# Kernel tuning notes

Measured on AMD Instinct MI355X. Metric: run time of the kernel, lower is better.

The kernel has to match this reference:

```python
import jax, jax.numpy as jnp
import numpy as np

S, B, R, H, TOP, CHL = 512, 32, 8, 128, 3, 19
I = CHL + 1  # GRU input size after null-channel concat


def setup_inputs() -> dict:
    key = jax.random.key(0)
    ks = jax.random.split(key, 12)
    f = lambda k, shp, sc=0.05: jax.random.normal(k, shp, dtype=jnp.float32) * sc
    return {
        "x": f(ks[0], (B, CHL, S), 1.0),
        "Wih": f(ks[1], (R, 3 * H, I)),      # per-rim GRU input weights (torch order r,z,n)
        "Whh": f(ks[2], (R, 3 * H, H)),      # per-rim GRU hidden weights
        "Qir_w": f(ks[3], (H, H)),
        "Qir_b": f(ks[4], (H,)),
        "Kir_w": f(ks[5], (H, S)),
        "Vir_w": f(ks[6], (H, S)),
        "Qrr_w": f(ks[7], (H, H)),
        "Krr_w": f(ks[8], (H, H)),
        "Vrr_w": f(ks[9], (H, H)),
    }


def reference(x, Wih, Whh, Qir_w, Qir_b, Kir_w, Vir_w, Qrr_w, Krr_w, Vrr_w):
    Bn = x.shape[0]
    # prepend null channel, reshape to (S, B, I)
    xc = jnp.concatenate([jnp.zeros((Bn, 1, x.shape[2]), x.dtype), x], axis=1)
    xs = jnp.transpose(xc, (2, 0, 1))  # (S, B, I)

    # ---- per-rim GRU (no bias), torch gate order (r, z, n) ----
    x_proj = jnp.einsum('sbi,rgi->srbg', xs, Wih)  # (S, R, B, 3H)

    def step(hprev, xp):
        hp = jnp.einsum('rbh,rgh->rbg', hprev, Whh)
        xr, xz, xn = jnp.split(xp, 3, axis=-1)
        hr, hz, hn = jnp.split(hp, 3, axis=-1)
        r = jax.nn.sigmoid(xr + hr)
        z = jax.nn.sigmoid(xz + hz)
        n = jnp.tanh(xn + r * hn)
        hnew = (1.0 - z) * n + z * hprev
        return hnew, hnew

    h0 = jnp.zeros((R, Bn, H), x.dtype)
    _, hs = jax.lax.scan(step, h0, x_proj)      # (S, R, B, H)
    h = jnp.transpose(hs, (1, 0, 2, 3))          # (R, S, B, H)

    # ---- stage one: input attention + rim competition ----
    x_bis = jnp.transpose(xs, (1, 2, 0))         # (B, I, S)
    q = jnp.einsum('rsbh,oh->rsbo', h, Qir_w) + Qir_b
    k = jnp.einsum('bis,os->bio', x_bis, Kir_w)
    v = jnp.einsum('bis,os->bio', x_bis, Vir_w)
    qk = jnp.einsum('rsbh,bih->sbri', q, k) / (H ** 0.5)
    soft = jax.nn.softmax(qk, axis=3)            # (S, B, R, I)
    idx = jax.lax.top_k(-soft[..., 0], TOP)[1]   # (S, B, TOP)
    mask = jnp.sum(jax.nn.one_hot(idx, R, dtype=jnp.float32), axis=-2)[..., None]  # (S,B,R,1)
    mask = jax.lax.stop_gradient(mask)
    qkv = jnp.einsum('sbri,bih->sbrh', soft, v)  # (S, B, R, H)

    # NoGrad: forward identity, backward grad*mask
    h1 = qkv * mask + jax.lax.stop_gradient(qkv * (1.0 - mask))

    # ---- stage two: rim-rim attention, masked ----
    q2 = jnp.einsum('sbrh,oh->sbro', h1, Qrr_w)
    k2 = jnp.einsum('sbrh,oh->sbro', h1, Krr_w)
    v2 = jnp.einsum('sbrh,oh->sbro', h1, Vrr_w)
    qk2 = jnp.einsum('sbrh,sbch->sbrc', q2, k2)  # (S, B, R, R), no scaling (as in source)
    soft2 = jax.nn.softmax(qk2, axis=3) * mask
    out = h1 + jnp.einsum('sbrc,sbch->sbrh', soft2, v2)
    return out * mask
```

## Files before the change

kernel.cpp:

```cpp
#include <hip/hip_runtime.h>
#include <math.h>


typedef float v2f __attribute__((ext_vector_type(2)));

#define PKF(acc, w, h) \
    asm("v_pk_fma_f32 %0, %1, %2, %0" : "+v"(acc) : "v"(w), "v"(h))

__global__ __launch_bounds__(256) void kPro1(const float* __restrict__ Kir,
        const float* __restrict__ Vir, const float* __restrict__ Vrr,
        const float* __restrict__ Qrr, const float* __restrict__ Krr,
        float* __restrict__ KirT, float* __restrict__ VirT,
        float* __restrict__ VrrT, float* __restrict__ M) {
    const int bid = blockIdx.x;
    if (bid < 576) {
        int idx = bid * 256 + threadIdx.x;
        if (idx < 65536) {
            int s = idx >> 7, o = idx & 127;
            KirT[idx] = Kir[o * 512 + s];
        } else if (idx < 131072) {
            int j = idx - 65536;
            int s = j >> 7, o = j & 127;
            VirT[j] = Vir[o * 512 + s];
        } else if (idx < 147456) {
            int j = idx - 131072;
            int g = j >> 7, h = j & 127;
            VrrT[j] = Vrr[h * 128 + g];
        }
    } else {
        const int h = (bid - 576) * 2 + (threadIdx.x >> 7);
        const int g = threadIdx.x & 127;
        float acc = 0.0f;
#pragma unroll 4
        for (int o = 0; o < 128; ++o) acc += Qrr[o * 128 + h] * Krr[o * 128 + g];
        M[h * 128 + g] = acc;
    }
}

__global__ __launch_bounds__(128) void kPro2(const float* __restrict__ x,
        const float* __restrict__ KirT, const float* __restrict__ VirT,
        const float* __restrict__ Qir, const float* __restrict__ Qib,
        float* __restrict__ vbuf, float* __restrict__ KQ, float* __restrict__ cb) {
    const int b = blockIdx.x / 20, i = blockIdx.x % 20;
    const int o = threadIdx.x;
    if (i == 0) {
        vbuf[(b * 20) * 128 + o] = 0.0f;
        KQ[(b * 20) * 128 + o] = 0.0f;
        if (o == 0) cb[b * 20] = 0.0f;
        return;
    }
    __shared__ float xL[512];
    __shared__ float kL[128];
    for (int idx = o; idx < 512; idx += 128)
        xL[idx] = x[(b * 19 + (i - 1)) * 512 + idx];
    __syncthreads();
    float ak = 0.0f, av = 0.0f;
#pragma unroll 4
    for (int s = 0; s < 512; ++s) {
        float xv = xL[s];
        ak += xv * KirT[s * 128 + o];
        av += xv * VirT[s * 128 + o];
    }
    vbuf[(b * 20 + i) * 128 + o] = av;
    kL[o] = ak;
    __syncthreads();
    float acc = 0.0f;
#pragma unroll 4
    for (int p = 0; p < 128; ++p) acc += kL[p] * Qir[p * 128 + o];
    KQ[(b * 20 + i) * 128 + o] = acc;
    if (o == 0) {
        float c = 0.0f;
        for (int p = 0; p < 128; ++p) c += kL[p] * Qib[p];
        cb[b * 20 + i] = c;
    }
}

template<int CTRL>
__device__ __forceinline__ float dppadd(float v) {
    int r = __builtin_amdgcn_update_dpp(0, __float_as_int(v), CTRL, 0xF, 0xF, true);
    return v + __int_as_float(r);
}
template<int CTRL>
__device__ __forceinline__ float dppbcast(float v) {
    int r = __builtin_amdgcn_update_dpp(0, __float_as_int(v), CTRL, 0xF, 0xF, true);
    return __int_as_float(r);
}

__global__ __launch_bounds__(512, 2) void kGRU(const float* __restrict__ x,
        const float* __restrict__ Wih, const float* __restrict__ Whh,
        float* __restrict__ hs) {
    const int r = blockIdx.x >> 5;
    const int b = blockIdx.x & 31;
    const int t = threadIdx.x;
    const int j = t >> 2;
    const int kq = t & 3;

    __shared__ __align__(16) float xT[512 * 20];
    __shared__ __align__(16) float hsBuf[64 * 144];

    for (int idx = t; idx < 19 * 512; idx += 512) {
        int c = idx >> 9, s = idx & 511;
        xT[s * 20 + c] = x[(b * 19 + c) * 512 + s];
    }
    if (t < 144) hsBuf[63 * 144 + t] = 0.0f;

    v2f w0[16], w1[16], w2[16];
    {
        const float* Wb = Whh + (r * 384) * 128 + kq * 32;
        const v2f* s0p = (const v2f*)(Wb + (j) * 128);
        const v2f* s1p = (const v2f*)(Wb + (j + 128) * 128);
        const v2f* s2p = (const v2f*)(Wb + (j + 256) * 128);
#pragma unroll
        for (int u = 0; u < 16; ++u) {
            w0[u] = s0p[u];
            w1[u] = s1p[u];
            w2[u] = s2p[u];
        }
    }
    v2f wiv[9];
    float wlast;
    if (kq < 3) {
        const float* W = Wih + (r * 384 + (j + 128 * kq)) * 20;
#pragma unroll
        for (int c = 0; c < 9; ++c) wiv[c] = (v2f){W[2*c + 1], W[2*c + 2]};
        wlast = W[19];
    } else {
#pragma unroll
        for (int c = 0; c < 9; ++c) wiv[c] = (v2f){0.0f, 0.0f};
        wlast = 0.0f;
    }
    __syncthreads();

    const int jmap = j + ((j >> 5) << 2);
    const int cellBase = (b * 8 + r) * 128;
    float hprev = 0.0f;

    for (int s = 0; s < 512; ++s) {
        const int rowR = (s + 63) & 63;
        const v2f* hp2 = (const v2f*)(hsBuf + rowR * 144 + kq * 36);
        v2f hv[16];
#pragma unroll
        for (int u = 0; u < 16; ++u) hv[u] = hp2[u];

        float xp;
        {
            const v2f* xp2 = (const v2f*)(xT + s * 20);
            float x18 = xT[s * 20 + 18];
            v2f xacc = {0.0f, 0.0f};
            PKF(xacc, wiv[0], xp2[0]);
            PKF(xacc, wiv[1], xp2[1]);
            PKF(xacc, wiv[2], xp2[2]);
            PKF(xacc, wiv[3], xp2[3]);
            PKF(xacc, wiv[4], xp2[4]);
            PKF(xacc, wiv[5], xp2[5]);
            PKF(xacc, wiv[6], xp2[6]);
            PKF(xacc, wiv[7], xp2[7]);
            PKF(xacc, wiv[8], xp2[8]);
            xp = xacc[0] + xacc[1] + wlast * x18;
        }

        v2f a0 = {0.0f, 0.0f}, a1 = {0.0f, 0.0f}, a2 = {0.0f, 0.0f};
#pragma unroll
        for (int u = 0; u < 16; ++u) {
            v2f hh = hv[u];
            PKF(a0, w0[u], hh);
            PKF(a1, w1[u], hh);
            PKF(a2, w2[u], hh);
        }
        float p0 = a0[0] + a0[1];
        float p1 = a1[0] + a1[1];
        float p2 = a2[0] + a2[1];

        p0 = dppadd<0xB1>(p0); p1 = dppadd<0xB1>(p1); p2 = dppadd<0xB1>(p2);
        p0 = dppadd<0x4E>(p0); p1 = dppadd<0x4E>(p1); p2 = dppadd<0x4E>(p2);
        float xr = dppbcast<0x00>(xp);
        float xz = dppbcast<0x55>(xp);
        float xn = dppbcast<0xAA>(xp);

        float rg = __builtin_amdgcn_rcpf(1.0f + __expf(-(p0 + xr)));
        float zg = __builtin_amdgcn_rcpf(1.0f + __expf(-(p1 + xz)));
        float a  = xn + rg * p2;
        float ng = 1.0f - 2.0f * __builtin_amdgcn_rcpf(__expf(2.0f * a) + 1.0f);
        float hnew = ng + zg * (hprev - ng);
        hprev = hnew;
        if (kq == 0) hsBuf[(s & 63) * 144 + jmap] = hnew;
        __syncthreads();

        if ((s & 63) == 63) {
            const int sBase = s - 63;
            const int c4 = (t & 31) * 4;
            const int cm = c4 + ((c4 >> 5) << 2);
#pragma unroll
            for (int w = 0; w < 4; ++w) {
                int rr = (t >> 5) + w * 16;
                float4 v = *(const float4*)(hsBuf + rr * 144 + cm);
                *(float4*)(hs + (size_t)(sBase + rr) * 32768 + cellBase + c4) = v;
            }
            __syncthreads();
        }
    }
}

__global__ __launch_bounds__(256) void kS1(const float* __restrict__ hs,
        const float* __restrict__ KQ, const float* __restrict__ cb,
        const float* __restrict__ vbuf,
        float* __restrict__ h1, int* __restrict__ widx, float* __restrict__ out) {
    const int b = blockIdx.x & 31;
    const int s0 = (blockIdx.x >> 5) * 8;
    const int t = threadIdx.x;
    __shared__ __align__(16) float KQL[20 * 132];
    __shared__ float vL[20 * 128];
    __shared__ float cbL[20];
    __shared__ __align__(16) float hLt[8 * 132];
    __shared__ float qkL[8 * 20];
    __shared__ float sfL[8 * 20];
    __shared__ float s0L[8];
    __shared__ int wselL[3];

    for (int idx = t; idx < 2560; idx += 256) {
        int i = idx >> 7, h = idx & 127;
        KQL[i * 132 + h] = KQ[(b * 20 + i) * 128 + h];
        vL[i * 128 + h] = vbuf[(b * 20 + i) * 128 + h];
    }
    if (t < 20) cbL[t] = cb[b * 20 + t];
    __syncthreads();

    for (int p = 0; p < 8; ++p) {
        const int s = s0 + p;
        {
            int r = t >> 5, h4 = t & 31;
            float4 hv = *(const float4*)(hs + ((s * 32 + b) * 8 + r) * 128 + h4 * 4);
            *(float4*)(hLt + r * 132 + h4 * 4) = hv;
        }
        __syncthreads();
        if (t < 152) {
            int r = t / 19, i = t % 19 + 1;
            const float4* hr4 = (const float4*)(hLt + r * 132);
            const float4* kg4 = (const float4*)(KQL + i * 132);
            float a = 0.0f;
#pragma unroll
            for (int q = 0; q < 32; ++q) {
                float4 hq = hr4[q];
                float4 kq = kg4[q];
                a += hq.x * kq.x;
                a += hq.y * kq.y;
                a += hq.z * kq.z;
                a += hq.w * kq.w;
            }
            qkL[r * 20 + i] = (a + cbL[i]) * 0.08838834764831845f;
        }
        if (t < 8) qkL[t * 20] = 0.0f;
        __syncthreads();
        if (t < 8) {
            float m = -3.4e38f;
            for (int i = 0; i < 20; ++i) m = fmaxf(m, qkL[t * 20 + i]);
            float sum = 0.0f;
            for (int i = 0; i < 20; ++i) {
                float e = expf(qkL[t * 20 + i] - m);
                sfL[t * 20 + i] = e;
                sum += e;
            }
            float inv = 1.0f / sum;
            for (int i = 0; i < 20; ++i) sfL[t * 20 + i] *= inv;
            s0L[t] = sfL[t * 20];
        }
        if (t == 0) {
            unsigned chosen = 0;
            for (int n = 0; n < 3; ++n) {
                float best = 3.4e38f; int bi = 0;
                for (int r2 = 0; r2 < 8; ++r2) {
                    if (chosen & (1u << r2)) continue;
                    float v = s0L[r2];
                    if (v < best) { best = v; bi = r2; }
                }
                chosen |= (1u << bi);
                wselL[n] = bi;
                widx[(s * 32 + b) * 3 + n] = bi;
            }
        }
        __syncthreads();
        {
            const int h = t & 127, rq = t >> 7;
            float a0 = 0, a1 = 0, a2 = 0, a3 = 0;
            for (int i = 1; i < 20; ++i) {
                float vv = vL[i * 128 + h];
                a0 += sfL[(rq * 4 + 0) * 20 + i] * vv;
                a1 += sfL[(rq * 4 + 1) * 20 + i] * vv;
                a2 += sfL[(rq * 4 + 2) * 20 + i] * vv;
                a3 += sfL[(rq * 4 + 3) * 20 + i] * vv;
            }
            const int pairBase = (s * 32 + b) * 8;
            float av[4] = {a0, a1, a2, a3};
#pragma unroll
            for (int jj = 0; jj < 4; ++jj) {
                int rim = rq * 4 + jj;
                h1[(pairBase + rim) * 128 + h] = av[jj];
                bool win = (wselL[0] == rim) || (wselL[1] == rim) || (wselL[2] == rim);
                if (!win) out[(pairBase + rim) * 128 + h] = 0.0f;
            }
        }
        __syncthreads();
    }
}

template<int EPI>
__global__ __launch_bounds__(256) void kGemm(
        const float* __restrict__ Asrc,
        const float* __restrict__ Bm,
        const int* __restrict__ widx,
        const float* __restrict__ h1g,
        float* __restrict__ C) {
    __shared__ float ALt[64][68];
    __shared__ float BL[64][128];
    const int n0 = blockIdx.x * 64;
    const int t = threadIdx.x;
    const int tr = t >> 4, tc = t & 15;
    const int q0 = 2 * tc, q1 = 2 * tc + 1;
    const int bq0 = (q0 ^ (q0 >> 3)) * 4;
    const int bq1 = (q1 ^ (q1 >> 3)) * 4;
    float acc[4][8];
#pragma unroll
    for (int i = 0; i < 4; ++i)
#pragma unroll
        for (int jj = 0; jj < 8; ++jj) acc[i][jj] = 0.0f;

    for (int kc = 0; kc < 128; kc += 64) {
        __syncthreads();
#pragma unroll
        for (int i = 0; i < 4; ++i) {
            int idx = t + i * 256;
            int row = idx >> 4, qk = idx & 15;
            const float* src;
            if (EPI == 0) {
                int n = n0 + row;
                int pair = n / 3;
                int rim = widx[n];
                src = Asrc + ((pair << 3) + rim) * 128 + kc + qk * 4;
            } else {
                src = Asrc + (n0 + row) * 128 + kc + qk * 4;
            }
            float4 a = *(const float4*)src;
            ALt[qk * 4 + 0][row] = a.x;
            ALt[qk * 4 + 1][row] = a.y;
            ALt[qk * 4 + 2][row] = a.z;
            ALt[qk * 4 + 3][row] = a.w;
        }
#pragma unroll
        for (int i = 0; i < 8; ++i) {
            int idx = t + i * 256;
            int kk = idx >> 5, qc = idx & 31;
            float4 bv = *(const float4*)(Bm + (kc + kk) * 128 + qc * 4);
            int pos = (qc ^ (qc >> 3)) * 4;
            *(float4*)&BL[kk][pos] = bv;
        }
        __syncthreads();
#pragma unroll 2
        for (int k = 0; k < 64; ++k) {
            float4 a0 = *(const float4*)&ALt[k][4 * tr];
            float4 b0 = *(const float4*)&BL[k][bq0];
            float4 b1 = *(const float4*)&BL[k][bq1];
            float ar[4] = {a0.x, a0.y, a0.z, a0.w};
            float bc[8] = {b0.x, b0.y, b0.z, b0.w, b1.x, b1.y, b1.z, b1.w};
#pragma unroll
            for (int i = 0; i < 4; ++i)
#pragma unroll
                for (int jj = 0; jj < 8; ++jj) acc[i][jj] += ar[i] * bc[jj];
        }
    }
    if (EPI == 0) {
#pragma unroll
        for (int i = 0; i < 4; ++i) {
            int row = n0 + 4 * tr + i;
            *(float4*)(C + row * 128 + 8 * tc) =
                make_float4(acc[i][0], acc[i][1], acc[i][2], acc[i][3]);
            *(float4*)(C + row * 128 + 8 * tc + 4) =
                make_float4(acc[i][4], acc[i][5], acc[i][6], acc[i][7]);
        }
    } else {
#pragma unroll
        for (int i = 0; i < 4; ++i) {
            int n = n0 + 4 * tr + i;
            int pair = n / 3;
            int rim = widx[n];
            int base = ((pair << 3) + rim) * 128 + 8 * tc;
            float4 w0 = *(const float4*)(h1g + base);
            float4 w1 = *(const float4*)(h1g + base + 4);
            *(float4*)(C + base) = make_float4(acc[i][0] + w0.x, acc[i][1] + w0.y,
                                               acc[i][2] + w0.z, acc[i][3] + w0.w);
            *(float4*)(C + base + 4) = make_float4(acc[i][4] + w1.x, acc[i][5] + w1.y,
                                                   acc[i][6] + w1.z, acc[i][7] + w1.w);
        }
    }
}

__global__ __launch_bounds__(256) void kS2c(const float* __restrict__ T1,
        const float* __restrict__ h1, float* __restrict__ U) {
    const int w = threadIdx.x >> 6;
    const int lane = threadIdx.x & 63;
    const int p = blockIdx.x * 4 + w;
    const int base8 = p * 8 * 128;
    float hv0[8], hv1[8];
#pragma unroll
    for (int c = 0; c < 8; ++c) {
        hv0[c] = h1[base8 + c * 128 + lane];
        hv1[c] = h1[base8 + c * 128 + 64 + lane];
    }
    float t0[3], t1v[3];
#pragma unroll
    for (int wr = 0; wr < 3; ++wr) {
        t0[wr]  = T1[(p * 3 + wr) * 128 + lane];
        t1v[wr] = T1[(p * 3 + wr) * 128 + 64 + lane];
    }
    float pr[3][8];
#pragma unroll
    for (int wr = 0; wr < 3; ++wr)
#pragma unroll
        for (int c = 0; c < 8; ++c)
            pr[wr][c] = t0[wr] * hv0[c] + t1v[wr] * hv1[c];
#pragma unroll
    for (int off = 32; off > 0; off >>= 1)
#pragma unroll
        for (int wr = 0; wr < 3; ++wr)
#pragma unroll
            for (int c = 0; c < 8; ++c)
                pr[wr][c] += __shfl_xor(pr[wr][c], off, 64);
#pragma unroll
    for (int wr = 0; wr < 3; ++wr) {
        float m = pr[wr][0];
#pragma unroll
        for (int c = 1; c < 8; ++c) m = fmaxf(m, pr[wr][c]);
        float sum = 0.0f;
#pragma unroll
        for (int c = 0; c < 8; ++c) { pr[wr][c] = expf(pr[wr][c] - m); sum += pr[wr][c]; }
        float inv = 1.0f / sum;
        float u0 = 0.0f, u1 = 0.0f;
#pragma unroll
        for (int c = 0; c < 8; ++c) {
            float sv = pr[wr][c] * inv;
            u0 += sv * hv0[c];
            u1 += sv * hv1[c];
        }
        U[(p * 3 + wr) * 128 + lane] = u0;
        U[(p * 3 + wr) * 128 + 64 + lane] = u1;
    }
}

extern "C" void kernel_launch(void* const* d_in, const int* in_sizes, int n_in,
                              void* d_out, int out_size, void* d_ws, size_t ws_size,
                              hipStream_t stream) {
    const float* x   = (const float*)d_in[0];
    const float* Wih = (const float*)d_in[1];
    const float* Whh = (const float*)d_in[2];
    const float* Qir = (const float*)d_in[3];
    const float* Qib = (const float*)d_in[4];
    const float* Kir = (const float*)d_in[5];
    const float* Vir = (const float*)d_in[6];
    const float* Qrr = (const float*)d_in[7];
    const float* Krr = (const float*)d_in[8];
    const float* Vrr = (const float*)d_in[9];
    float* out = (float*)d_out;
    float* ws  = (float*)d_ws;

    float* hs   = ws;
    float* h1   = ws + 16777216;
    float* KirT = ws + 33554432;
    float* VirT = ws + 33619968;
    float* VrrT = ws + 33685504;
    float* vb   = ws + 33783808;
    float* KQ   = ws + 33865728;
    float* cb   = ws + 33947648;
    float* Mm   = ws + 33948288;
    int*   widx = (int*)(ws + 33964672);
    float* T1   = ws;
    float* U    = ws + 6291456;

    (void)in_sizes; (void)n_in; (void)out_size; (void)ws_size;

    kPro1<<<640, 256, 0, stream>>>(Kir, Vir, Vrr, Qrr, Krr, KirT, VirT, VrrT, Mm);
    kPro2<<<640, 128, 0, stream>>>(x, KirT, VirT, Qir, Qib, vb, KQ, cb);
    kGRU <<<256, 512, 0, stream>>>(x, Wih, Whh, hs);
    kS1  <<<2048, 256, 0, stream>>>(hs, KQ, cb, vb, h1, widx, out);
    kGemm<0><<<768, 256, 0, stream>>>(h1, Mm, widx, nullptr, T1);
    kS2c <<<4096, 256, 0, stream>>>(T1, h1, U);
    kGemm<1><<<768, 256, 0, stream>>>(U, VrrT, widx, h1, out);
}
```

Baseline: 534.6 us.

## Fuse stage-two GEMMs and softmax into one per-pair kernel

Replaces the three stage-two launches (gather GEMM with Qrr^T·Krr, per-pair softmax and weighting, GEMM with Vrr plus residual) with one kernel. Each wave handles four (s,b) pairs and stages the winning rims' h1 rows in shared memory. It computes the projections with per-lane weight rows read straight from global memory, then applies softmax and the Vrr product in registers. This removes the T1/U intermediate round trips and two launches. In exchange it gives up the tiled shared-memory GEMM reuse: every wave re-reads the full 128x128 MT and Vrr matrices from cache, with strided float4 per-lane loads.

```diff
diff --git a/kernel.cpp b/kernel.cpp
--- a/kernel.cpp
+++ b/kernel.cpp
@@ -8,32 +8,28 @@
     asm("v_pk_fma_f32 %0, %1, %2, %0" : "+v"(acc) : "v"(w), "v"(h))
 
 __global__ __launch_bounds__(256) void kPro1(const float* __restrict__ Kir,
-        const float* __restrict__ Vir, const float* __restrict__ Vrr,
+        const float* __restrict__ Vir,
         const float* __restrict__ Qrr, const float* __restrict__ Krr,
         float* __restrict__ KirT, float* __restrict__ VirT,
-        float* __restrict__ VrrT, float* __restrict__ M) {
+        float* __restrict__ MT) {
     const int bid = blockIdx.x;
-    if (bid < 576) {
+    if (bid < 512) {
         int idx = bid * 256 + threadIdx.x;
         if (idx < 65536) {
             int s = idx >> 7, o = idx & 127;
             KirT[idx] = Kir[o * 512 + s];
-        } else if (idx < 131072) {
+        } else {
             int j = idx - 65536;
             int s = j >> 7, o = j & 127;
             VirT[j] = Vir[o * 512 + s];
-        } else if (idx < 147456) {
-            int j = idx - 131072;
-            int g = j >> 7, h = j & 127;
-            VrrT[j] = Vrr[h * 128 + g];
         }
     } else {
-        const int h = (bid - 576) * 2 + (threadIdx.x >> 7);
-        const int g = threadIdx.x & 127;
+        const int g = (bid - 512) * 2 + (threadIdx.x >> 7);
+        const int h = threadIdx.x & 127;
         float acc = 0.0f;
 #pragma unroll 4
         for (int o = 0; o < 128; ++o) acc += Qrr[o * 128 + h] * Krr[o * 128 + g];
-        M[h * 128 + g] = acc;
+        MT[g * 128 + h] = acc;
     }
 }
 
@@ -303,146 +299,119 @@
     }
 }
 
-template<int EPI>
-__global__ __launch_bounds__(256) void kGemm(
-        const float* __restrict__ Asrc,
-        const float* __restrict__ Bm,
-        const int* __restrict__ widx,
-        const float* __restrict__ h1g,
-        float* __restrict__ C) {
-    __shared__ float ALt[64][68];
-    __shared__ float BL[64][128];
-    const int n0 = blockIdx.x * 64;
-    const int t = threadIdx.x;
-    const int tr = t >> 4, tc = t & 15;
-    const int q0 = 2 * tc, q1 = 2 * tc + 1;
-    const int bq0 = (q0 ^ (q0 >> 3)) * 4;
-    const int bq1 = (q1 ^ (q1 >> 3)) * 4;
-    float acc[4][8];
-#pragma unroll
-    for (int i = 0; i < 4; ++i)
-#pragma unroll
-        for (int jj = 0; jj < 8; ++jj) acc[i][jj] = 0.0f;
-
-    for (int kc = 0; kc < 128; kc += 64) {
-        __syncthreads();
-#pragma unroll
-        for (int i = 0; i < 4; ++i) {
-            int idx = t + i * 256;
-            int row = idx >> 4, qk = idx & 15;
-            const float* src;
-            if (EPI == 0) {
-                int n = n0 + row;
-                int pair = n / 3;
-                int rim = widx[n];
-                src = Asrc + ((pair << 3) + rim) * 128 + kc + qk * 4;
-            } else {
-                src = Asrc + (n0 + row) * 128 + kc + qk * 4;
-            }
-            float4 a = *(const float4*)src;
-            ALt[qk * 4 + 0][row] = a.x;
-            ALt[qk * 4 + 1][row] = a.y;
-            ALt[qk * 4 + 2][row] = a.z;
-            ALt[qk * 4 + 3][row] = a.w;
-        }
-#pragma unroll
-        for (int i = 0; i < 8; ++i) {
-            int idx = t + i * 256;
-            int kk = idx >> 5, qc = idx & 31;
-            float4 bv = *(const float4*)(Bm + (kc + kk) * 128 + qc * 4);
-            int pos = (qc ^ (qc >> 3)) * 4;
-            *(float4*)&BL[kk][pos] = bv;
-        }
-        __syncthreads();
+__global__ __launch_bounds__(256) void kS2G(const float* __restrict__ h1,
+        const int* __restrict__ widx, const float* __restrict__ MT,
+        const float* __restrict__ Vrr, float* __restrict__ out) {
+    const int wv = threadIdx.x >> 6;
+    const int lane = threadIdx.x & 63;
+    const int p0 = blockIdx.x * 16 + wv * 4;
+    __shared__ __align__(16) float scr[4][1536];
+    float* S = scr[wv];
+
+    int wq[4][3];
+#pragma unroll
+    for (int q = 0; q < 4; ++q)
+#pragma unroll
+        for (int wr = 0; wr < 3; ++wr)
+            wq[q][wr] = widx[(p0 + q) * 3 + wr];
+
+#pragma unroll
+    for (int q = 0; q < 4; ++q)
+#pragma unroll
+        for (int wr = 0; wr < 3; ++wr) {
+            const float* src = h1 + ((p0 + q) * 8 + wq[q][wr]) * 128;
+            S[(q * 3 + wr) * 128 + lane] = src[lane];
+            S[(q * 3 + wr) * 128 + 64 + lane] = src[64 + lane];
+        }
+
+    float a0[4][3], a1[4][3];
+#pragma unroll
+    for (int q = 0; q < 4; ++q)
+#pragma unroll
+        for (int wr = 0; wr < 3; ++wr) { a0[q][wr] = 0.0f; a1[q][wr] = 0.0f; }
 #pragma unroll 2
-        for (int k = 0; k < 64; ++k) {
-            float4 a0 = *(const float4*)&ALt[k][4 * tr];
-            float4 b0 = *(const float4*)&BL[k][bq0];
-            float4 b1 = *(const float4*)&BL[k][bq1];
-            float ar[4] = {a0.x, a0.y, a0.z, a0.w};
-            float bc[8] = {b0.x, b0.y, b0.z, b0.w, b1.x, b1.y, b1.z, b1.w};
-#pragma unroll
-            for (int i = 0; i < 4; ++i)
-#pragma unroll
-                for (int jj = 0; jj < 8; ++jj) acc[i][jj] += ar[i] * bc[jj];
-        }
-    }
-    if (EPI == 0) {
-#pragma unroll
-        for (int i = 0; i < 4; ++i) {
-            int row = n0 + 4 * tr + i;
-            *(float4*)(C + row * 128 + 8 * tc) =
-                make_float4(acc[i][0], acc[i][1], acc[i][2], acc[i][3]);
-            *(float4*)(C + row * 128 + 8 * tc + 4) =
-                make_float4(acc[i][4], acc[i][5], acc[i][6], acc[i][7]);
-        }
-    } else {
-#pragma unroll
-        for (int i = 0; i < 4; ++i) {
-            int n = n0 + 4 * tr + i;
-            int pair = n / 3;
-            int rim = widx[n];
-            int base = ((pair << 3) + rim) * 128 + 8 * tc;
-            float4 w0 = *(const float4*)(h1g + base);
-            float4 w1 = *(const float4*)(h1g + base + 4);
-            *(float4*)(C + base) = make_float4(acc[i][0] + w0.x, acc[i][1] + w0.y,
-                                               acc[i][2] + w0.z, acc[i][3] + w0.w);
-            *(float4*)(C + base + 4) = make_float4(acc[i][4] + w1.x, acc[i][5] + w1.y,
-                                                   acc[i][6] + w1.z, acc[i][7] + w1.w);
-        }
-    }
-}
-
-__global__ __launch_bounds__(256) void kS2c(const float* __restrict__ T1,
-        const float* __restrict__ h1, float* __restrict__ U) {
-    const int w = threadIdx.x >> 6;
-    const int lane = threadIdx.x & 63;
-    const int p = blockIdx.x * 4 + w;
-    const int base8 = p * 8 * 128;
-    float hv0[8], hv1[8];
-#pragma unroll
-    for (int c = 0; c < 8; ++c) {
-        hv0[c] = h1[base8 + c * 128 + lane];
-        hv1[c] = h1[base8 + c * 128 + 64 + lane];
-    }
-    float t0[3], t1v[3];
-#pragma unroll
-    for (int wr = 0; wr < 3; ++wr) {
-        t0[wr]  = T1[(p * 3 + wr) * 128 + lane];
-        t1v[wr] = T1[(p * 3 + wr) * 128 + 64 + lane];
-    }
-    float pr[3][8];
-#pragma unroll
-    for (int wr = 0; wr < 3; ++wr)
-#pragma unroll
-        for (int c = 0; c < 8; ++c)
-            pr[wr][c] = t0[wr] * hv0[c] + t1v[wr] * hv1[c];
-#pragma unroll
-    for (int off = 32; off > 0; off >>= 1)
+    for (int h4 = 0; h4 < 128; h4 += 4) {
+        float4 ma = *(const float4*)(MT + lane * 128 + h4);
+        float4 mb = *(const float4*)(MT + (lane + 64) * 128 + h4);
+#pragma unroll
+        for (int q = 0; q < 4; ++q)
+#pragma unroll
+            for (int wr = 0; wr < 3; ++wr) {
+                float4 u4 = *(const float4*)(S + (q * 3 + wr) * 128 + h4);
+                a0[q][wr] += u4.x * ma.x + u4.y * ma.y + u4.z * ma.z + u4.w * ma.w;
+                a1[q][wr] += u4.x * mb.x + u4.y * mb.y + u4.z * mb.z + u4.w * mb.w;
+            }
+    }
+
+#pragma unroll
+    for (int q = 0; q < 4; ++q) {
+        float hv0[8], hv1[8];
+        const float* hp = h1 + (p0 + q) * 8 * 128;
+#pragma unroll
+        for (int c = 0; c < 8; ++c) {
+            hv0[c] = hp[c * 128 + lane];
+            hv1[c] = hp[c * 128 + 64 + lane];
+        }
+        float pr[3][8];
 #pragma unroll
         for (int wr = 0; wr < 3; ++wr)
 #pragma unroll
             for (int c = 0; c < 8; ++c)
-                pr[wr][c] += __shfl_xor(pr[wr][c], off, 64);
-#pragma unroll
-    for (int wr = 0; wr < 3; ++wr) {
-        float m = pr[wr][0];
-#pragma unroll
-        for (int c = 1; c < 8; ++c) m = fmaxf(m, pr[wr][c]);
-        float sum = 0.0f;
-#pragma unroll
-        for (int c = 0; c < 8; ++c) { pr[wr][c] = expf(pr[wr][c] - m); sum += pr[wr][c]; }
-        float inv = 1.0f / sum;
-        float u0 = 0.0f, u1 = 0.0f;
-#pragma unroll
-        for (int c = 0; c < 8; ++c) {
-            float sv = pr[wr][c] * inv;
-            u0 += sv * hv0[c];
-            u1 += sv * hv1[c];
-        }
-        U[(p * 3 + wr) * 128 + lane] = u0;
-        U[(p * 3 + wr) * 128 + 64 + lane] = u1;
-    }
+                pr[wr][c] = a0[q][wr] * hv0[c] + a1[q][wr] * hv1[c];
+#pragma unroll
+        for (int off = 32; off > 0; off >>= 1)
+#pragma unroll
+            for (int wr = 0; wr < 3; ++wr)
+#pragma unroll
+                for (int c = 0; c < 8; ++c)
+                    pr[wr][c] += __shfl_xor(pr[wr][c], off, 64);
+#pragma unroll
+        for (int wr = 0; wr < 3; ++wr) {
+            float m = pr[wr][0];
+#pragma unroll
+            for (int c = 1; c < 8; ++c) m = fmaxf(m, pr[wr][c]);
+            float sum = 0.0f;
+#pragma unroll
+            for (int c = 0; c < 8; ++c) { pr[wr][c] = expf(pr[wr][c] - m); sum += pr[wr][c]; }
+            float inv = 1.0f / sum;
+            float uu0 = 0.0f, uu1 = 0.0f;
+#pragma unroll
+            for (int c = 0; c < 8; ++c) {
+                float sv = pr[wr][c] * inv;
+                uu0 += sv * hv0[c];
+                uu1 += sv * hv1[c];
+            }
+            S[(q * 3 + wr) * 128 + lane] = uu0;
+            S[(q * 3 + wr) * 128 + 64 + lane] = uu1;
+        }
+    }
+
+    float b0[4][3], b1[4][3];
+#pragma unroll
+    for (int q = 0; q < 4; ++q)
+#pragma unroll
+        for (int wr = 0; wr < 3; ++wr) { b0[q][wr] = 0.0f; b1[q][wr] = 0.0f; }
+#pragma unroll 2
+    for (int g4 = 0; g4 < 128; g4 += 4) {
+        float4 va = *(const float4*)(Vrr + lane * 128 + g4);
+        float4 vb = *(const float4*)(Vrr + (lane + 64) * 128 + g4);
+#pragma unroll
+        for (int q = 0; q < 4; ++q)
+#pragma unroll
+            for (int wr = 0; wr < 3; ++wr) {
+                float4 u4 = *(const float4*)(S + (q * 3 + wr) * 128 + g4);
+                b0[q][wr] += u4.x * va.x + u4.y * va.y + u4.z * va.z + u4.w * va.w;
+                b1[q][wr] += u4.x * vb.x + u4.y * vb.y + u4.z * vb.z + u4.w * vb.w;
+            }
+    }
+#pragma unroll
+    for (int q = 0; q < 4; ++q)
+#pragma unroll
+        for (int wr = 0; wr < 3; ++wr) {
+            const int base = ((p0 + q) * 8 + wq[q][wr]) * 128;
+            out[base + lane] = h1[base + lane] + b0[q][wr];
+            out[base + 64 + lane] = h1[base + 64 + lane] + b1[q][wr];
+        }
 }
 
 extern "C" void kernel_launch(void* const* d_in, const int* in_sizes, int n_in,
@@ -465,22 +434,17 @@
     float* h1   = ws + 16777216;
     float* KirT = ws + 33554432;
     float* VirT = ws + 33619968;
-    float* VrrT = ws + 33685504;
     float* vb   = ws + 33783808;
     float* KQ   = ws + 33865728;
     float* cb   = ws + 33947648;
-    float* Mm   = ws + 33948288;
+    float* MT   = ws + 33948288;
     int*   widx = (int*)(ws + 33964672);
-    float* T1   = ws;
-    float* U    = ws + 6291456;
 
     (void)in_sizes; (void)n_in; (void)out_size; (void)ws_size;
 
-    kPro1<<<640, 256, 0, stream>>>(Kir, Vir, Vrr, Qrr, Krr, KirT, VirT, VrrT, Mm);
+    kPro1<<<576, 256, 0, stream>>>(Kir, Vir, Qrr, Krr, KirT, VirT, MT);
     kPro2<<<640, 128, 0, stream>>>(x, KirT, VirT, Qir, Qib, vb, KQ, cb);
     kGRU <<<256, 512, 0, stream>>>(x, Wih, Whh, hs);
     kS1  <<<2048, 256, 0, stream>>>(hs, KQ, cb, vb, h1, widx, out);
-    kGemm<0><<<768, 256, 0, stream>>>(h1, Mm, widx, nullptr, T1);
-    kS2c <<<4096, 256, 0, stream>>>(T1, h1, U);
-    kGemm<1><<<768, 256, 0, stream>>>(U, VrrT, widx, h1, out);
-}
+    kS2G <<<1024, 256, 0, stream>>>(h1, widx, MT, Vrr, out);
+}
```

After: 542.2 us. Within noise of the previous version (+1.4%).
